# Kernel optimization log

Measured on AMD Instinct MI355X. Metric: run time of the kernel, lower is better.

The kernel has to match this reference:

```python
import jax, jax.numpy as jnp
import numpy as np

NUM_HEADS = 16
HEAD_DIM = 64  # hidden_size 1024 / 16 heads


def setup_inputs() -> dict:
    key = jax.random.key(0)
    ks = jax.random.split(key, 7)
    B, S, D = 32, 577, 1024
    s = 0.02
    return {
        "hidden_states": jax.random.normal(ks[0], (B, S, D), dtype=jnp.float32),
        "Wq": jax.random.normal(ks[1], (D, D), dtype=jnp.float32) * s,
        "bq": jax.random.normal(ks[2], (D,), dtype=jnp.float32) * s,
        "Wk": jax.random.normal(ks[3], (D, D), dtype=jnp.float32) * s,
        "bk": jax.random.normal(ks[4], (D,), dtype=jnp.float32) * s,
        "Wv": jax.random.normal(ks[5], (D, D), dtype=jnp.float32) * s,
        "bv": jax.random.normal(ks[6], (D,), dtype=jnp.float32) * s,
    }


def _split_heads(x):
    # [B, S, D] -> [B, H, S, d]
    B, S, D = x.shape
    return x.reshape(B, S, NUM_HEADS, HEAD_DIM).transpose(0, 2, 1, 3)


def reference(hidden_states, Wq, bq, Wk, bk, Wv, bv):
    # torch Linear: y = x @ W^T + b
    q = _split_heads(hidden_states @ Wq.T + bq)  # [B,H,S,d]
    k = _split_heads(hidden_states @ Wk.T + bk)
    v = _split_heads(hidden_states @ Wv.T + bv)

    scale = 1.0 / np.sqrt(HEAD_DIM).astype(np.float32)
    scores = jnp.einsum("bhqd,bhkd->bhqk", q, k) * scale  # [B,H,S,S]
    probs = jax.nn.softmax(scores, axis=-1)
    ctx = jnp.einsum("bhqk,bhkd->bhqd", probs, v)  # [B,H,S,d]
    B, H, S, d = ctx.shape
    ctx = ctx.transpose(0, 2, 1, 3).reshape(B, S, H * d)  # [B,S,D]
    return ctx
```

## Files before the change

kernel.cpp:

```cpp
#include <hip/hip_runtime.h>
#include <stdint.h>

#define NB 32
#define SEQ 577
#define SPAD 640
#define NH 16
#define HD 64
#define DM 1024
#define MTOT (NB * SEQ)
#define KT_N 16

typedef __bf16 bf16x8 __attribute__((ext_vector_type(8)));
typedef float f32x4 __attribute__((ext_vector_type(4)));
typedef unsigned short u16x8 __attribute__((ext_vector_type(8)));
typedef unsigned short u16x4 __attribute__((ext_vector_type(4)));

__device__ __forceinline__ unsigned short f2bf(float f) {
  unsigned int u = __builtin_bit_cast(unsigned int, f);
  return (unsigned short)((u + 0x7FFFu + ((u >> 16) & 1u)) >> 16);
}

__device__ __forceinline__ f32x4 mfma16(bf16x8 a, bf16x8 b, f32x4 c) {
  return __builtin_amdgcn_mfma_f32_16x16x32_bf16(a, b, c, 0, 0, 0);
}

__device__ __forceinline__ void gload16(const unsigned short* g, unsigned short* l) {
  __builtin_amdgcn_global_load_lds(
      (const __attribute__((address_space(1))) unsigned int*)g,
      (__attribute__((address_space(3))) unsigned int*)l, 16, 0, 0);
}

#define BC8(p) __builtin_bit_cast(bf16x8, *(const u16x8*)(p))

#if __has_builtin(__builtin_amdgcn_exp2f)
#define EXP2(x) __builtin_amdgcn_exp2f(x)
#else
#define EXP2(x) exp2f(x)
#endif

__global__ void cvt_kernel(const float* __restrict__ x,
                           const float* __restrict__ wq,
                           const float* __restrict__ wk,
                           const float* __restrict__ wv,
                           unsigned short* __restrict__ xb,
                           unsigned short* __restrict__ wb) {
  const long long NX = (long long)MTOT * DM;
  long long i = ((long long)blockIdx.x * blockDim.x + threadIdx.x) * 4;
  const float* src;
  unsigned short* dst;
  if (i < NX) {
    src = x + i;
    dst = xb + i;
  } else {
    long long j = i - NX;
    int wsel = (int)(j >> 20);
    long long off = j & 0xFFFFF;
    src = (wsel == 0 ? wq : wsel == 1 ? wk : wv) + off;
    dst = wb + j;
  }
  f32x4 v = *(const f32x4*)src;
  u16x4 o;
  o.x = f2bf(v.x); o.y = f2bf(v.y); o.z = f2bf(v.z); o.w = f2bf(v.w);
  *(u16x4*)dst = o;
}

__global__ __launch_bounds__(512, 2) void qk_gemm8(
    const unsigned short* __restrict__ xb, const unsigned short* __restrict__ wb,
    const float* __restrict__ bq, const float* __restrict__ bk,
    unsigned short* __restrict__ qo, unsigned short* __restrict__ ko) {
  __shared__ __align__(16) unsigned short LDS[65536];
  const int id = blockIdx.x;
  const int xcd = id & 7;
  const int idx = id >> 3;
  const int z = xcd >> 2;
  const int n0 = (xcd & 3) * 256;
  const int m0 = idx * 256;

  const int t = threadIdx.x;
  const int lane = t & 63;
  const int w = t >> 6;
  const int g = lane >> 4, c = lane & 15;
  const int wm = w & 1, wn = w >> 1;

  const unsigned short* W = wb + (size_t)z * (DM * DM);
  const float* bias = z ? bk : bq;
  unsigned short* outp = z ? ko : qo;

  const int srow = t >> 3;
  const int schunk = (t & 7) ^ (srow & 7);
  const unsigned short* gA[4];
#pragma unroll
  for (int q = 0; q < 4; q++) {
    int rg = m0 + q * 64 + srow;
    if (rg > MTOT - 1) rg = MTOT - 1;
    gA[q] = xb + (size_t)rg * DM + schunk * 8;
  }
  const unsigned short* gB[4];
#pragma unroll
  for (int q = 0; q < 4; q++)
    gB[q] = W + (size_t)(n0 + q * 64 + srow) * DM + schunk * 8;

  const int cx = c & 7;
  const int ch0 = (g ^ cx) * 8;
  const int ch1 = ((4 + g) ^ cx) * 8;

  f32x4 acc[8][4];
#pragma unroll
  for (int mi = 0; mi < 8; mi++)
#pragma unroll
    for (int ni = 0; ni < 4; ni++) acc[mi][ni] = (f32x4)0.0f;

#pragma unroll
  for (int q = 0; q < 4; q++) gload16(gA[q], LDS + q * 4096 + t * 8);
#pragma unroll
  for (int q = 0; q < 4; q++) gload16(gB[q], LDS + 16384 + q * 4096 + t * 8);
#pragma unroll
  for (int q = 0; q < 4; q++) gload16(gA[q] + 64, LDS + 32768 + q * 4096 + t * 8);
#pragma unroll
  for (int q = 0; q < 4; q++)
    gload16(gB[q] + 64, LDS + 32768 + 16384 + q * 4096 + t * 8);
  asm volatile("s_waitcnt vmcnt(8)" ::: "memory");
  __builtin_amdgcn_sched_barrier(0);
  __builtin_amdgcn_s_barrier();

  const int rA0 = wm * 128 + c;
  const int rB0 = wn * 64 + c;

  for (int kt = 0; kt < KT_N; ++kt) {
    unsigned short* ab = LDS + (kt & 1) * 32768;
    unsigned short* bb = ab + 16384;
    const bool st = (kt + 2) < KT_N;
    const int ko2 = (kt + 2) * 64;
    bf16x8 af[4][2], bf0[2][2], bf1[2][2];

#pragma unroll
    for (int mi = 0; mi < 4; mi++) {
      const unsigned short* rp = ab + (rA0 + mi * 16) * 64;
      af[mi][0] = BC8(rp + ch0);
      af[mi][1] = BC8(rp + ch1);
    }
#pragma unroll
    for (int ni = 0; ni < 2; ni++) {
      const unsigned short* rp = bb + (rB0 + ni * 16) * 64;
      bf0[ni][0] = BC8(rp + ch0);
      bf0[ni][1] = BC8(rp + ch1);
    }
    __builtin_amdgcn_s_barrier();
    asm volatile("s_waitcnt lgkmcnt(0)" ::: "memory");
    __builtin_amdgcn_sched_barrier(0);
    __builtin_amdgcn_s_setprio(1);
#pragma unroll
    for (int mi = 0; mi < 4; mi++)
#pragma unroll
      for (int ni = 0; ni < 2; ni++) {
        acc[mi][ni] = mfma16(af[mi][0], bf0[ni][0], acc[mi][ni]);
        acc[mi][ni] = mfma16(af[mi][1], bf0[ni][1], acc[mi][ni]);
      }
    __builtin_amdgcn_s_setprio(0);
    __builtin_amdgcn_s_barrier();

#pragma unroll
    for (int ni = 0; ni < 2; ni++) {
      const unsigned short* rp = bb + (rB0 + (2 + ni) * 16) * 64;
      bf1[ni][0] = BC8(rp + ch0);
      bf1[ni][1] = BC8(rp + ch1);
    }
    if (st) {
      gload16(gA[0] + ko2, ab + 0 * 4096 + t * 8);
      gload16(gA[2] + ko2, ab + 2 * 4096 + t * 8);
    }
    __builtin_amdgcn_s_barrier();
    asm volatile("s_waitcnt lgkmcnt(0)" ::: "memory");
    __builtin_amdgcn_sched_barrier(0);
    __builtin_amdgcn_s_setprio(1);
#pragma unroll
    for (int mi = 0; mi < 4; mi++)
#pragma unroll
      for (int ni = 0; ni < 2; ni++) {
        acc[mi][2 + ni] = mfma16(af[mi][0], bf1[ni][0], acc[mi][2 + ni]);
        acc[mi][2 + ni] = mfma16(af[mi][1], bf1[ni][1], acc[mi][2 + ni]);
      }
    __builtin_amdgcn_s_setprio(0);
    __builtin_amdgcn_s_barrier();

#pragma unroll
    for (int mi = 0; mi < 4; mi++) {
      const unsigned short* rp = ab + (rA0 + 64 + mi * 16) * 64;
      af[mi][0] = BC8(rp + ch0);
      af[mi][1] = BC8(rp + ch1);
    }
    if (st) {
#pragma unroll
      for (int q = 0; q < 4; q++) gload16(gB[q] + ko2, bb + q * 4096 + t * 8);
    }
    __builtin_amdgcn_s_barrier();
    asm volatile("s_waitcnt lgkmcnt(0)" ::: "memory");
    __builtin_amdgcn_sched_barrier(0);
    __builtin_amdgcn_s_setprio(1);
#pragma unroll
    for (int mi = 0; mi < 4; mi++)
#pragma unroll
      for (int ni = 0; ni < 2; ni++) {
        acc[4 + mi][2 + ni] = mfma16(af[mi][0], bf1[ni][0], acc[4 + mi][2 + ni]);
        acc[4 + mi][2 + ni] = mfma16(af[mi][1], bf1[ni][1], acc[4 + mi][2 + ni]);
      }
    __builtin_amdgcn_s_setprio(0);
    __builtin_amdgcn_s_barrier();

    if (st) {
      gload16(gA[1] + ko2, ab + 1 * 4096 + t * 8);
      gload16(gA[3] + ko2, ab + 3 * 4096 + t * 8);
    }
    __builtin_amdgcn_s_barrier();
    __builtin_amdgcn_s_setprio(1);
#pragma unroll
    for (int mi = 0; mi < 4; mi++)
#pragma unroll
      for (int ni = 0; ni < 2; ni++) {
        acc[4 + mi][ni] = mfma16(af[mi][0], bf0[ni][0], acc[4 + mi][ni]);
        acc[4 + mi][ni] = mfma16(af[mi][1], bf0[ni][1], acc[4 + mi][ni]);
      }
    __builtin_amdgcn_s_setprio(0);
    asm volatile("s_waitcnt vmcnt(8)" ::: "memory");
    __builtin_amdgcn_sched_barrier(0);
    __builtin_amdgcn_s_barrier();
  }

  float bias4[4];
#pragma unroll
  for (int ni = 0; ni < 4; ni++) bias4[ni] = bias[n0 + wn * 64 + ni * 16 + c];

#pragma unroll
  for (int mi = 0; mi < 8; mi++) {
    int mb = m0 + wm * 128 + mi * 16 + g * 4;
#pragma unroll
    for (int r = 0; r < 4; r++) {
      int m = mb + r;
      if (m >= MTOT) continue;
      int bi = m / SEQ;
      int s = m - bi * SEQ;
#pragma unroll
      for (int ni = 0; ni < 4; ni++) {
        int n = n0 + wn * 64 + ni * 16 + c;
        int hh = n >> 6, dd = n & 63;
        outp[(((size_t)bi * NH + hh) * SPAD + s) * HD + dd] =
            f2bf(acc[mi][ni][r] + bias4[ni]);
      }
    }
  }
}

__global__ __launch_bounds__(256, 2) void vt_gemm(
    const unsigned short* __restrict__ xb, const unsigned short* __restrict__ wb,
    const float* __restrict__ bv, unsigned short* __restrict__ vo) {
  const int id = blockIdx.x;
  const int xcd = id & 7;
  const int m_tile = id >> 3;
  const int n0 = xcd * 128;
  const int m0 = m_tile * 128;

  __shared__ __align__(16) unsigned short As[128 * 32];
  __shared__ __align__(16) unsigned short Bs[128 * 32];
  const int t = threadIdx.x;
  const unsigned short* W = wb + (size_t)2 * (DM * DM);

  const int lane = t & 63;
  const int g = lane >> 4, c = lane & 15;
  const int w = t >> 6;
  const int wm = w & 1, wn = w >> 1;

  const int srow = t >> 2;
  const int scol = (t & 3) * 8;
  int ar0 = m0 + srow;      if (ar0 > MTOT - 1) ar0 = MTOT - 1;
  int ar1 = m0 + 64 + srow; if (ar1 > MTOT - 1) ar1 = MTOT - 1;
  const unsigned short* gA0 = xb + (size_t)ar0 * DM + scol;
  const unsigned short* gA1 = xb + (size_t)ar1 * DM + scol;
  const unsigned short* gB0 = W + (size_t)(n0 + srow) * DM + scol;
  const unsigned short* gB1 = W + (size_t)(n0 + 64 + srow) * DM + scol;
  unsigned short* lA0 = As + t * 8;
  unsigned short* lA1 = As + 2048 + t * 8;
  unsigned short* lB0 = Bs + t * 8;
  unsigned short* lB1 = Bs + 2048 + t * 8;

  f32x4 acc[4][4];
#pragma unroll
  for (int mi = 0; mi < 4; mi++)
#pragma unroll
    for (int ni = 0; ni < 4; ni++) acc[mi][ni] = (f32x4)0.0f;

  for (int k0 = 0; k0 < DM; k0 += 32) {
    __syncthreads();
    gload16(gA0 + k0, lA0);
    gload16(gA1 + k0, lA1);
    gload16(gB0 + k0, lB0);
    gload16(gB1 + k0, lB1);
    __syncthreads();
    bf16x8 af[4], bfr[4];
#pragma unroll
    for (int mi = 0; mi < 4; mi++)
      af[mi] = __builtin_bit_cast(
          bf16x8, *(const u16x8*)(As + (wm * 64 + mi * 16 + c) * 32 + g * 8));
#pragma unroll
    for (int ni = 0; ni < 4; ni++)
      bfr[ni] = __builtin_bit_cast(
          bf16x8, *(const u16x8*)(Bs + (wn * 64 + ni * 16 + c) * 32 + g * 8));
#pragma unroll
    for (int mi = 0; mi < 4; mi++)
#pragma unroll
      for (int ni = 0; ni < 4; ni++)
        acc[mi][ni] = mfma16(bfr[ni], af[mi], acc[mi][ni]);
  }

#pragma unroll
  for (int ni = 0; ni < 4; ni++) {
#pragma unroll
    for (int r = 0; r < 4; r++) {
      int n = n0 + wn * 64 + ni * 16 + g * 4 + r;
      int hh = n >> 6, dd = n & 63;
      float bn = bv[n];
#pragma unroll
      for (int mi = 0; mi < 4; mi++) {
        int m = m0 + wm * 64 + mi * 16 + c;
        if (m >= MTOT) continue;
        int bi = m / SEQ;
        int s = m - bi * SEQ;
        vo[(((size_t)bi * NH + hh) * HD + dd) * SPAD + s] =
            f2bf(acc[mi][ni][r] + bn);
      }
    }
  }
}

__global__ __launch_bounds__(256, 4) void attn_kernel(
    const unsigned short* __restrict__ Qb, const unsigned short* __restrict__ Kb,
    const unsigned short* __restrict__ Vt, float* __restrict__ out) {
  __shared__ __align__(16) unsigned short Ks[64 * 64];
  __shared__ __align__(16) unsigned short Vs[80 * 64];
  __shared__ __align__(16) unsigned short Pl[4][16 * 72];
  const int t = threadIdx.x, lane = t & 63, w = t >> 6;
  const int g = lane >> 4, c = lane & 15;

  const int id = blockIdx.x;
  const int xcd = id & 7;
  const int slot = id >> 3;
  const int qt = slot % 10;
  const int pairIdx = slot / 10;
  const int pair = xcd * 64 + pairIdx;
  const int b = pair >> 4;
  const int h = pair & 15;

  const int q0 = qt * 64 + w * 16;
  const size_t bh = (size_t)b * NH + h;
  const unsigned short* Qp = Qb + bh * SPAD * HD;
  const unsigned short* Kp = Kb + bh * SPAD * HD;
  const unsigned short* Vp = Vt + bh * HD * SPAD;

  {
    int rr = t >> 4, col = (t & 15) * 4;
    unsigned short val = (rr == 0) ? (unsigned short)0x3F80 : (unsigned short)0;
    u16x4 v4 = {val, val, val, val};
    *(u16x4*)(Vs + (64 + rr) * 64 + col) = v4;
  }

  bf16x8 qf0 = __builtin_bit_cast(
      bf16x8, *(const u16x8*)(Qp + (size_t)(q0 + c) * HD + g * 8));
  bf16x8 qf1 = __builtin_bit_cast(
      bf16x8, *(const u16x8*)(Qp + (size_t)(q0 + c) * HD + 32 + g * 8));

  const int C0 = t, C1 = t + 256;
  const int r0 = C0 >> 3, cg0 = (C0 & 7) ^ (r0 & 7);
  const int r1 = C1 >> 3, cg1 = (C1 & 7) ^ (r1 & 7);
  const unsigned short* gK0 = Kp + (size_t)(r0 * 8 + cg0) * 8;
  const unsigned short* gK1 = Kp + (size_t)(r1 * 8 + cg1) * 8;
  const unsigned short* gV0 = Vp + (size_t)r0 * SPAD + cg0 * 8;
  const unsigned short* gV1 = Vp + (size_t)r1 * SPAD + cg1 * 8;
  unsigned short* lK0 = Ks + C0 * 8;
  unsigned short* lK1 = Ks + C1 * 8;
  unsigned short* lV0 = Vs + C0 * 8;
  unsigned short* lV1 = Vs + C1 * 8;

  f32x4 oacc[5];
#pragma unroll
  for (int nt = 0; nt < 5; nt++) oacc[nt] = (f32x4)0.0f;
  unsigned short* pl = &Pl[w][0];
  const float SC = 0.125f * 1.44269504f;

  for (int kt = 0; kt < 10; kt++) {
    const int kv0 = kt * 64;
    __syncthreads();
    gload16(gK0 + kv0 * 64, lK0);
    gload16(gK1 + kv0 * 64, lK1);
    gload16(gV0 + kv0, lV0);
    gload16(gV1 + kv0, lV1);
    __syncthreads();

    f32x4 sc[4];
#pragma unroll
    for (int nt = 0; nt < 4; nt++) {
      const int row = nt * 16 + c;
      const unsigned short* kb = Ks + row * 64;
      bf16x8 k0 = __builtin_bit_cast(
          bf16x8, *(const u16x8*)(kb + ((g ^ (row & 7)) * 8)));
      bf16x8 k1 = __builtin_bit_cast(
          bf16x8, *(const u16x8*)(kb + (((4 + g) ^ (row & 7)) * 8)));
      sc[nt] = mfma16(qf0, k0, (f32x4)0.0f);
      sc[nt] = mfma16(qf1, k1, sc[nt]);
    }

    if (kt == 9) {
#pragma unroll
      for (int nt = 0; nt < 4; nt++) {
        const bool valid = (kv0 + nt * 16 + c) < SEQ;
#pragma unroll
        for (int r = 0; r < 4; r++)
          sc[nt][r] = valid ? EXP2(sc[nt][r] * SC) : 0.0f;
      }
    } else {
#pragma unroll
      for (int nt = 0; nt < 4; nt++)
#pragma unroll
        for (int r = 0; r < 4; r++) sc[nt][r] = EXP2(sc[nt][r] * SC);
    }

#pragma unroll
    for (int nt = 0; nt < 4; nt++)
#pragma unroll
      for (int r = 0; r < 4; r++)
        pl[(g * 4 + r) * 72 + nt * 16 + c] = f2bf(sc[nt][r]);
    bf16x8 pa0 = __builtin_bit_cast(bf16x8, *(const u16x8*)(pl + c * 72 + g * 8));
    bf16x8 pa1 =
        __builtin_bit_cast(bf16x8, *(const u16x8*)(pl + c * 72 + 32 + g * 8));

#pragma unroll
    for (int nt = 0; nt < 5; nt++) {
      const int row = nt * 16 + c;
      const unsigned short* vb = Vs + row * 64;
      bf16x8 v0 = __builtin_bit_cast(
          bf16x8, *(const u16x8*)(vb + ((g ^ (row & 7)) * 8)));
      bf16x8 v1 = __builtin_bit_cast(
          bf16x8, *(const u16x8*)(vb + (((4 + g) ^ (row & 7)) * 8)));
      oacc[nt] = mfma16(pa0, v0, oacc[nt]);
      oacc[nt] = mfma16(pa1, v1, oacc[nt]);
    }
  }

#pragma unroll
  for (int r = 0; r < 4; r++) {
    int s = q0 + g * 4 + r;
    if (s >= SEQ) continue;
    float l = __shfl(oacc[4][r], lane & 48, 64);
    float inv = 1.0f / l;
#pragma unroll
    for (int nt = 0; nt < 4; nt++)
      out[((size_t)b * SEQ + s) * DM + h * HD + nt * 16 + c] =
          oacc[nt][r] * inv;
  }
}

extern "C" void kernel_launch(void* const* d_in, const int* in_sizes, int n_in,
                              void* d_out, int out_size, void* d_ws,
                              size_t ws_size, hipStream_t stream) {
  const float* x = (const float*)d_in[0];
  const float* Wq = (const float*)d_in[1];
  const float* bq = (const float*)d_in[2];
  const float* Wk = (const float*)d_in[3];
  const float* bk = (const float*)d_in[4];
  const float* Wv = (const float*)d_in[5];
  const float* bv = (const float*)d_in[6];
  float* out = (float*)d_out;

  const size_t nXB = (size_t)MTOT * DM;
  const size_t nWB = (size_t)3 * DM * DM;
  const size_t nQK = (size_t)NB * NH * SPAD * HD;
  const size_t needed = (nXB + nWB + 3 * nQK) * 2;
  if (ws_size < needed) return;

  unsigned short* xb = (unsigned short*)d_ws;
  unsigned short* wb = xb + nXB;
  unsigned short* Qb = wb + nWB;
  unsigned short* Kb = Qb + nQK;
  unsigned short* Vt = Kb + nQK;

  cvt_kernel<<<21536, 256, 0, stream>>>(x, Wq, Wk, Wv, xb, wb);
  qk_gemm8<<<584, 512, 0, stream>>>(xb, wb, bq, bk, Qb, Kb);
  vt_gemm<<<1160, 256, 0, stream>>>(xb, wb, bv, Vt);
  attn_kernel<<<5120, 256, 0, stream>>>(Qb, Kb, Vt, out);
}
```

Measured before the change: 414.7 us.

## Unify Q/K/V projections into templated 256x256 pipelined GEMM with XCD-aware tile mapping

The simple 128x128 V-transpose GEMM is replaced by a template mode of the pipelined 256x256 GEMM, which swaps MFMA operands so the V output can be written transposed. Block-to-tile mapping is reworked so each XCD covers a contiguous range of M tiles, aiming for better L2 reuse of activation rows. Several intermediate s_barriers in the main loop are removed and global prefetches are issued before the LDS fragment reads to increase overlap. Fewer barriers risk LDS hazards if the remaining synchronisation is not enough, and the V kernel now launches only 292 large blocks.

```diff
diff --git a/kernel.cpp b/kernel.cpp
--- a/kernel.cpp
+++ b/kernel.cpp
@@ -64,17 +64,31 @@
   *(u16x4*)dst = o;
 }
 
-__global__ __launch_bounds__(512, 2) void qk_gemm8(
+template <int MODE>
+__global__ __launch_bounds__(512, 2) void gemm256(
     const unsigned short* __restrict__ xb, const unsigned short* __restrict__ wb,
     const float* __restrict__ bq, const float* __restrict__ bk,
-    unsigned short* __restrict__ qo, unsigned short* __restrict__ ko) {
+    const float* __restrict__ bv,
+    unsigned short* __restrict__ qo, unsigned short* __restrict__ ko,
+    unsigned short* __restrict__ vo) {
   __shared__ __align__(16) unsigned short LDS[65536];
   const int id = blockIdx.x;
-  const int xcd = id & 7;
-  const int idx = id >> 3;
-  const int z = xcd >> 2;
-  const int n0 = (xcd & 3) * 256;
-  const int m0 = idx * 256;
+  int m_tile, col, z;
+  if constexpr (MODE == 0) {
+    const int xcd = id & 7, j = id >> 3;
+    const int p = xcd * 73 + j;
+    m_tile = p >> 3;
+    col = p & 7;
+    z = col >> 2;
+  } else {
+    const int xcd = id & 7, j = id >> 3;
+    const int p = (xcd < 4) ? xcd * 37 + j : 148 + (xcd - 4) * 36 + j;
+    m_tile = p >> 2;
+    col = p & 3;
+    z = 2;
+  }
+  const int n0 = (MODE == 0 ? (col & 3) : col) * 256;
+  const int m0 = m_tile * 256;
 
   const int t = threadIdx.x;
   const int lane = t & 63;
@@ -83,8 +97,8 @@
   const int wm = w & 1, wn = w >> 1;
 
   const unsigned short* W = wb + (size_t)z * (DM * DM);
-  const float* bias = z ? bk : bq;
-  unsigned short* outp = z ? ko : qo;
+  const float* bias = (MODE == 1) ? bv : (z ? bk : bq);
+  unsigned short* outp = (MODE == 1) ? vo : (z ? ko : qo);
 
   const int srow = t >> 3;
   const int schunk = (t & 7) ^ (srow & 7);
@@ -125,6 +139,14 @@
 
   const int rA0 = wm * 128 + c;
   const int rB0 = wn * 64 + c;
+
+#define MM(ACC, AF, BF)                                   \
+  do {                                                    \
+    if constexpr (MODE == 0)                              \
+      ACC = mfma16(AF, BF, ACC);                          \
+    else                                                  \
+      ACC = mfma16(BF, AF, ACC);                          \
+  } while (0)
 
   for (int kt = 0; kt < KT_N; ++kt) {
     unsigned short* ab = LDS + (kt & 1) * 32768;
@@ -145,7 +167,6 @@
       bf0[ni][0] = BC8(rp + ch0);
       bf0[ni][1] = BC8(rp + ch1);
     }
-    __builtin_amdgcn_s_barrier();
     asm volatile("s_waitcnt lgkmcnt(0)" ::: "memory");
     __builtin_amdgcn_sched_barrier(0);
     __builtin_amdgcn_s_setprio(1);
@@ -153,23 +174,22 @@
     for (int mi = 0; mi < 4; mi++)
 #pragma unroll
       for (int ni = 0; ni < 2; ni++) {
-        acc[mi][ni] = mfma16(af[mi][0], bf0[ni][0], acc[mi][ni]);
-        acc[mi][ni] = mfma16(af[mi][1], bf0[ni][1], acc[mi][ni]);
+        MM(acc[mi][ni], af[mi][0], bf0[ni][0]);
+        MM(acc[mi][ni], af[mi][1], bf0[ni][1]);
       }
     __builtin_amdgcn_s_setprio(0);
     __builtin_amdgcn_s_barrier();
 
+    if (st) {
+      gload16(gA[0] + ko2, ab + 0 * 4096 + t * 8);
+      gload16(gA[2] + ko2, ab + 2 * 4096 + t * 8);
+    }
 #pragma unroll
     for (int ni = 0; ni < 2; ni++) {
       const unsigned short* rp = bb + (rB0 + (2 + ni) * 16) * 64;
       bf1[ni][0] = BC8(rp + ch0);
       bf1[ni][1] = BC8(rp + ch1);
     }
-    if (st) {
-      gload16(gA[0] + ko2, ab + 0 * 4096 + t * 8);
-      gload16(gA[2] + ko2, ab + 2 * 4096 + t * 8);
-    }
-    __builtin_amdgcn_s_barrier();
     asm volatile("s_waitcnt lgkmcnt(0)" ::: "memory");
     __builtin_amdgcn_sched_barrier(0);
     __builtin_amdgcn_s_setprio(1);
@@ -177,23 +197,22 @@
     for (int mi = 0; mi < 4; mi++)
 #pragma unroll
       for (int ni = 0; ni < 2; ni++) {
-        acc[mi][2 + ni] = mfma16(af[mi][0], bf1[ni][0], acc[mi][2 + ni]);
-        acc[mi][2 + ni] = mfma16(af[mi][1], bf1[ni][1], acc[mi][2 + ni]);
+        MM(acc[mi][2 + ni], af[mi][0], bf1[ni][0]);
+        MM(acc[mi][2 + ni], af[mi][1], bf1[ni][1]);
       }
     __builtin_amdgcn_s_setprio(0);
     __builtin_amdgcn_s_barrier();
 
+    if (st) {
+#pragma unroll
+      for (int q = 0; q < 4; q++) gload16(gB[q] + ko2, bb + q * 4096 + t * 8);
+    }
 #pragma unroll
     for (int mi = 0; mi < 4; mi++) {
       const unsigned short* rp = ab + (rA0 + 64 + mi * 16) * 64;
       af[mi][0] = BC8(rp + ch0);
       af[mi][1] = BC8(rp + ch1);
     }
-    if (st) {
-#pragma unroll
-      for (int q = 0; q < 4; q++) gload16(gB[q] + ko2, bb + q * 4096 + t * 8);
-    }
-    __builtin_amdgcn_s_barrier();
     asm volatile("s_waitcnt lgkmcnt(0)" ::: "memory");
     __builtin_amdgcn_sched_barrier(0);
     __builtin_amdgcn_s_setprio(1);
@@ -201,8 +220,8 @@
     for (int mi = 0; mi < 4; mi++)
 #pragma unroll
       for (int ni = 0; ni < 2; ni++) {
-        acc[4 + mi][2 + ni] = mfma16(af[mi][0], bf1[ni][0], acc[4 + mi][2 + ni]);
-        acc[4 + mi][2 + ni] = mfma16(af[mi][1], bf1[ni][1], acc[4 + mi][2 + ni]);
+        MM(acc[4 + mi][2 + ni], af[mi][0], bf1[ni][0]);
+        MM(acc[4 + mi][2 + ni], af[mi][1], bf1[ni][1]);
       }
     __builtin_amdgcn_s_setprio(0);
     __builtin_amdgcn_s_barrier();
@@ -211,121 +230,60 @@
       gload16(gA[1] + ko2, ab + 1 * 4096 + t * 8);
       gload16(gA[3] + ko2, ab + 3 * 4096 + t * 8);
     }
-    __builtin_amdgcn_s_barrier();
     __builtin_amdgcn_s_setprio(1);
 #pragma unroll
     for (int mi = 0; mi < 4; mi++)
 #pragma unroll
       for (int ni = 0; ni < 2; ni++) {
-        acc[4 + mi][ni] = mfma16(af[mi][0], bf0[ni][0], acc[4 + mi][ni]);
-        acc[4 + mi][ni] = mfma16(af[mi][1], bf0[ni][1], acc[4 + mi][ni]);
+        MM(acc[4 + mi][ni], af[mi][0], bf0[ni][0]);
+        MM(acc[4 + mi][ni], af[mi][1], bf0[ni][1]);
       }
     __builtin_amdgcn_s_setprio(0);
     asm volatile("s_waitcnt vmcnt(8)" ::: "memory");
     __builtin_amdgcn_sched_barrier(0);
     __builtin_amdgcn_s_barrier();
   }
-
-  float bias4[4];
-#pragma unroll
-  for (int ni = 0; ni < 4; ni++) bias4[ni] = bias[n0 + wn * 64 + ni * 16 + c];
-
-#pragma unroll
-  for (int mi = 0; mi < 8; mi++) {
-    int mb = m0 + wm * 128 + mi * 16 + g * 4;
-#pragma unroll
-    for (int r = 0; r < 4; r++) {
-      int m = mb + r;
-      if (m >= MTOT) continue;
-      int bi = m / SEQ;
-      int s = m - bi * SEQ;
-#pragma unroll
-      for (int ni = 0; ni < 4; ni++) {
-        int n = n0 + wn * 64 + ni * 16 + c;
-        int hh = n >> 6, dd = n & 63;
-        outp[(((size_t)bi * NH + hh) * SPAD + s) * HD + dd] =
-            f2bf(acc[mi][ni][r] + bias4[ni]);
-      }
-    }
-  }
-}
-
-__global__ __launch_bounds__(256, 2) void vt_gemm(
-    const unsigned short* __restrict__ xb, const unsigned short* __restrict__ wb,
-    const float* __restrict__ bv, unsigned short* __restrict__ vo) {
-  const int id = blockIdx.x;
-  const int xcd = id & 7;
-  const int m_tile = id >> 3;
-  const int n0 = xcd * 128;
-  const int m0 = m_tile * 128;
-
-  __shared__ __align__(16) unsigned short As[128 * 32];
-  __shared__ __align__(16) unsigned short Bs[128 * 32];
-  const int t = threadIdx.x;
-  const unsigned short* W = wb + (size_t)2 * (DM * DM);
-
-  const int lane = t & 63;
-  const int g = lane >> 4, c = lane & 15;
-  const int w = t >> 6;
-  const int wm = w & 1, wn = w >> 1;
-
-  const int srow = t >> 2;
-  const int scol = (t & 3) * 8;
-  int ar0 = m0 + srow;      if (ar0 > MTOT - 1) ar0 = MTOT - 1;
-  int ar1 = m0 + 64 + srow; if (ar1 > MTOT - 1) ar1 = MTOT - 1;
-  const unsigned short* gA0 = xb + (size_t)ar0 * DM + scol;
-  const unsigned short* gA1 = xb + (size_t)ar1 * DM + scol;
-  const unsigned short* gB0 = W + (size_t)(n0 + srow) * DM + scol;
-  const unsigned short* gB1 = W + (size_t)(n0 + 64 + srow) * DM + scol;
-  unsigned short* lA0 = As + t * 8;
-  unsigned short* lA1 = As + 2048 + t * 8;
-  unsigned short* lB0 = Bs + t * 8;
-  unsigned short* lB1 = Bs + 2048 + t * 8;
-
-  f32x4 acc[4][4];
-#pragma unroll
-  for (int mi = 0; mi < 4; mi++)
-#pragma unroll
-    for (int ni = 0; ni < 4; ni++) acc[mi][ni] = (f32x4)0.0f;
-
-  for (int k0 = 0; k0 < DM; k0 += 32) {
-    __syncthreads();
-    gload16(gA0 + k0, lA0);
-    gload16(gA1 + k0, lA1);
-    gload16(gB0 + k0, lB0);
-    gload16(gB1 + k0, lB1);
-    __syncthreads();
-    bf16x8 af[4], bfr[4];
-#pragma unroll
-    for (int mi = 0; mi < 4; mi++)
-      af[mi] = __builtin_bit_cast(
-          bf16x8, *(const u16x8*)(As + (wm * 64 + mi * 16 + c) * 32 + g * 8));
-#pragma unroll
-    for (int ni = 0; ni < 4; ni++)
-      bfr[ni] = __builtin_bit_cast(
-          bf16x8, *(const u16x8*)(Bs + (wn * 64 + ni * 16 + c) * 32 + g * 8));
-#pragma unroll
-    for (int mi = 0; mi < 4; mi++)
-#pragma unroll
-      for (int ni = 0; ni < 4; ni++)
-        acc[mi][ni] = mfma16(bfr[ni], af[mi], acc[mi][ni]);
-  }
-
-#pragma unroll
-  for (int ni = 0; ni < 4; ni++) {
-#pragma unroll
-    for (int r = 0; r < 4; r++) {
-      int n = n0 + wn * 64 + ni * 16 + g * 4 + r;
-      int hh = n >> 6, dd = n & 63;
-      float bn = bv[n];
-#pragma unroll
-      for (int mi = 0; mi < 4; mi++) {
-        int m = m0 + wm * 64 + mi * 16 + c;
+#undef MM
+
+  if constexpr (MODE == 0) {
+    float bias4[4];
+#pragma unroll
+    for (int ni = 0; ni < 4; ni++) bias4[ni] = bias[n0 + wn * 64 + ni * 16 + c];
+#pragma unroll
+    for (int mi = 0; mi < 8; mi++) {
+      int mb = m0 + wm * 128 + mi * 16 + g * 4;
+#pragma unroll
+      for (int r = 0; r < 4; r++) {
+        int m = mb + r;
         if (m >= MTOT) continue;
         int bi = m / SEQ;
         int s = m - bi * SEQ;
-        vo[(((size_t)bi * NH + hh) * HD + dd) * SPAD + s] =
-            f2bf(acc[mi][ni][r] + bn);
+#pragma unroll
+        for (int ni = 0; ni < 4; ni++) {
+          int n = n0 + wn * 64 + ni * 16 + c;
+          int hh = n >> 6, dd = n & 63;
+          outp[(((size_t)bi * NH + hh) * SPAD + s) * HD + dd] =
+              f2bf(acc[mi][ni][r] + bias4[ni]);
+        }
+      }
+    }
+  } else {
+#pragma unroll
+    for (int ni = 0; ni < 4; ni++) {
+#pragma unroll
+      for (int r = 0; r < 4; r++) {
+        int n = n0 + wn * 64 + ni * 16 + g * 4 + r;
+        int hh = n >> 6, dd = n & 63;
+        float bn = bias[n];
+#pragma unroll
+        for (int mi = 0; mi < 8; mi++) {
+          int m = m0 + wm * 128 + mi * 16 + c;
+          if (m >= MTOT) continue;
+          int bi = m / SEQ;
+          int s = m - bi * SEQ;
+          outp[(((size_t)bi * NH + hh) * HD + dd) * SPAD + s] =
+              f2bf(acc[mi][ni][r] + bn);
+        }
       }
     }
   }
@@ -482,7 +440,7 @@
   unsigned short* Vt = Kb + nQK;
 
   cvt_kernel<<<21536, 256, 0, stream>>>(x, Wq, Wk, Wv, xb, wb);
-  qk_gemm8<<<584, 512, 0, stream>>>(xb, wb, bq, bk, Qb, Kb);
-  vt_gemm<<<1160, 256, 0, stream>>>(xb, wb, bv, Vt);
+  gemm256<0><<<584, 512, 0, stream>>>(xb, wb, bq, bk, bv, Qb, Kb, Vt);
+  gemm256<1><<<292, 512, 0, stream>>>(xb, wb, bq, bk, bv, Qb, Kb, Vt);
   attn_kernel<<<5120, 256, 0, stream>>>(Qb, Kb, Vt, out);
 }
```

After: 418.2 us. Within noise of the previous version (+0.8%).
